# Performance work log

Hardware: AMD Instinct MI355X
Metric: run time of the kernel (lower is better)

## Reference

```python
import jax, jax.numpy as jnp
import numpy as np

N = 100000   # users
E = 50000    # hyperedges per timestep
NNZ = 800000 # incidences per timestep
T = 8        # step_split
D = 64       # embed_dim


def setup_inputs() -> dict:
    key = jax.random.key(0)
    ks = jax.random.split(key, 9)
    s = 1.0 / np.sqrt(D)
    return {
        "user_emb": jax.random.normal(ks[0], (N, D), jnp.float32) * s,
        "W_conv": jax.random.normal(ks[1], (D, D), jnp.float32) * s,
        "b_conv": jnp.zeros((D,), jnp.float32),
        "fus_w1": jax.random.normal(ks[2], (D, D), jnp.float32) * s,
        "fus_b1": jnp.zeros((D,), jnp.float32),
        "fus_w2": jax.random.normal(ks[3], (D, 1), jnp.float32) * s,
        "fus_b2": jnp.zeros((1,), jnp.float32),
        "edge_nodes": jax.random.randint(ks[4], (T, NNZ), 0, N),
        "edge_hyper": jax.random.randint(ks[5], (T, NNZ), 0, E),
    }


def _hconv(h, nodes, hyper):
    # h: [N, D] transformed node feats; nodes/hyper: [NNZ] incidence list
    ones = jnp.ones((nodes.shape[0], 1), h.dtype)
    e_sum = jax.ops.segment_sum(h[nodes], hyper, num_segments=E)      # [E, D]
    e_cnt = jax.ops.segment_sum(ones, hyper, num_segments=E)          # [E, 1]
    e = e_sum / jnp.maximum(e_cnt, 1.0)
    n_sum = jax.ops.segment_sum(e[hyper], nodes, num_segments=N)      # [N, D]
    n_cnt = jax.ops.segment_sum(ones, nodes, num_segments=N)          # [N, 1]
    return n_sum / jnp.maximum(n_cnt, 1.0)


def _fuse(hidden, dy, w1, b1, w2, b2):
    emb = jnp.stack([hidden, dy], axis=0)                             # [2, N, D]
    score = jax.nn.softmax(jnp.tanh(emb @ w1 + b1) @ w2 + b2, axis=0)  # [2, N, 1]
    return jnp.sum(score * emb, axis=0)                                # [N, D]


def reference(user_emb, W_conv, b_conv, fus_w1, fus_b1, fus_w2, fus_b2,
              edge_nodes, edge_hyper):
    # Conv input is always the raw user embedding table -> per-step convs independent.
    h = jax.nn.relu(user_emb @ W_conv + b_conv)                        # [N, D]
    conv_out = jax.vmap(lambda nd, hy: _hconv(h, nd, hy))(edge_nodes, edge_hyper)  # [T, N, D]

    def step(carry, dy):
        out = _fuse(carry, dy, fus_w1, fus_b1, fus_w2, fus_b2)
        return out, None

    final, _ = jax.lax.scan(step, conv_out[0], conv_out[1:])
    return final
```

## Files before the change

kernel.cpp:

```cpp
#include <hip/hip_runtime.h>
#include <hip/hip_bf16.h>

#define N_USERS 100000
#define E_HYPER 50000
#define NNZ_E   800000
#define T_STEPS 8
#define DIM     64

#define CAP_E   64
#define CAP_N   44

#define TR_BLOCKS  1024
#define GE_BLOCKS  1563
#define GNF_BLOCKS 1563
#define ZERO_BLKS  147

#define SC_PARTS   8
#define SC_SUB     256
#define SC_BLOCKS  (SC_PARTS * SC_SUB)
#define SC_CHUNK   (NNZ_E / SC_SUB)
#define E_SLICE    (E_HYPER / SC_PARTS)
#define N_SLICE    (N_USERS / SC_PARTS)

typedef __bf16 bf16x8 __attribute__((ext_vector_type(8)));
typedef float  f32x4  __attribute__((ext_vector_type(4)));

__device__ __forceinline__ float ld_in(const void* p, size_t i, int f32)
{
    return f32 ? ((const float*)p)[i]
               : __bfloat162float(((const __hip_bfloat16*)p)[i]);
}

__device__ __forceinline__ void st_carry(void* out, float* cws, size_t i,
                                         int f, int use_ws, float v)
{
    if (f) { ((float*)out)[i] = v; return; }
    if (use_ws) { cws[i] = v; return; }
    ((__hip_bfloat16*)out)[i] = __float2bfloat16(v);
}

__global__ void k_detect(const unsigned short* __restrict__ raw, int* __restrict__ flag)
{
    __shared__ int cnt;
    if (threadIdx.x == 0) cnt = 0;
    __syncthreads();
    int c = 0;
    for (int i = threadIdx.x; i < 4096; i += blockDim.x) {
        int e = (raw[i] >> 7) & 0xFF;
        if (e > 126) c++;
    }
    atomicAdd(&cnt, c);
    __syncthreads();
    if (threadIdx.x == 0) *flag = (cnt > 64) ? 1 : 0;
}

__global__ void k_convert_params(
    const void* W, const void* b, const void* w1, const void* b1,
    const void* w2, const void* b2, const int* __restrict__ flag,
    float* __restrict__ st)
{
    int f = *flag;
    int i = blockIdx.x * blockDim.x + threadIdx.x;
    if (i < 4096)          st[i] = ld_in(W,  i,        f);
    else if (i < 4160)     st[i] = ld_in(b,  i - 4096, f);
    else if (i < 8256)     st[i] = ld_in(w1, i - 4160, f);
    else if (i < 8320)     st[i] = ld_in(b1, i - 8256, f);
    else if (i < 8384)     st[i] = ld_in(w2, i - 8320, f);
    else if (i == 8384)    st[i] = ld_in(b2, 0,        f);
}

__device__ __forceinline__ void appendE_body(
    const int* __restrict__ nodes, const int* __restrict__ hyper,
    int* __restrict__ cnt, int* __restrict__ sn_pad, int bid, int tid)
{
    int part = bid & (SC_PARTS - 1);
    int sub  = bid >> 3;
    int elo  = part * E_SLICE;
    int i0   = sub * SC_CHUNK;
    for (int i = i0 + tid; i < i0 + SC_CHUNK; i += 256) {
        int hy = hyper[i];
        if ((unsigned)(hy - elo) < (unsigned)E_SLICE) {
            int r = atomicAdd(&cnt[hy], 1);
            if (r < CAP_E) sn_pad[hy * CAP_E + r] = nodes[i];
        }
    }
}

__device__ __forceinline__ void appendN_body(
    const int* __restrict__ nodes, const int* __restrict__ hyper,
    int* __restrict__ cnt, int* __restrict__ sh_pad, int bid, int tid)
{
    int part = bid & (SC_PARTS - 1);
    int sub  = bid >> 3;
    int nlo  = part * N_SLICE;
    int i0   = sub * SC_CHUNK;
    for (int i = i0 + tid; i < i0 + SC_CHUNK; i += 256) {
        int nd = nodes[i];
        if ((unsigned)(nd - nlo) < (unsigned)N_SLICE) {
            int r = atomicAdd(&cnt[E_HYPER + nd], 1);
            if (r < CAP_N) sh_pad[nd * CAP_N + r] = hyper[i];
        }
    }
}

__device__ __forceinline__ void zero_body(int* __restrict__ buf, int b, int tid)
{
    int idx = b * 256 + tid;
    if (idx < 150000 / 4) ((int4*)buf)[idx] = make_int4(0, 0, 0, 0);
}

__device__ __forceinline__ void ge_body(
    const __hip_bfloat16* __restrict__ h,
    const int* __restrict__ sn_pad, const int* __restrict__ cnt_e,
    __hip_bfloat16* __restrict__ e, int bid, int tid)
{
    int lane = tid & 63;
    int wid = bid * 4 + (tid >> 6);
    int nW  = GE_BLOCKS * 4;
    for (int s0 = wid * 8; s0 < E_HYPER; s0 += nW * 8) {
        int pos[8], end8[8], cnt8[8]; float acc[8];
#pragma unroll
        for (int c = 0; c < 8; ++c) {
            int sg = s0 + c;
            int cc = (sg < E_HYPER) ? cnt_e[sg] : 0;
            cnt8[c] = cc;
            pos[c]  = sg * CAP_E;
            end8[c] = pos[c] + min(cc, CAP_E);
            acc[c]  = 0.f;
        }
        while (true) {
            bool any = false;
#pragma unroll
            for (int c = 0; c < 8; ++c) any = any || (pos[c] < end8[c]);
            if (!any) break;
            int id[8];
#pragma unroll
            for (int c = 0; c < 8; ++c)
                if (pos[c] < end8[c]) id[c] = sn_pad[pos[c]];
#pragma unroll
            for (int c = 0; c < 8; ++c)
                if (pos[c] < end8[c]) {
                    acc[c] += __bfloat162float(h[(size_t)id[c] * DIM + lane]);
                    pos[c]++;
                }
        }
#pragma unroll
        for (int c = 0; c < 8; ++c) {
            int sg = s0 + c;
            if (sg < E_HYPER)
                e[(size_t)sg * DIM + lane] =
                    __float2bfloat16(acc[c] / (float)max(cnt8[c], 1));
        }
    }
}

__device__ __forceinline__ void fu_tile(
    void* __restrict__ dout, float* __restrict__ cws,
    const float* __restrict__ dyl_t, const float* __restrict__ st,
    int f, int use_ws, int write_out, int row0, int tid)
{
    float* cf = f ? (float*)dout : (use_ws ? cws : (float*)0);
    __hip_bfloat16* cb = (__hip_bfloat16*)dout;

    int lane = tid & 63;
    int quad = lane >> 4;
    int m    = lane & 15;

    bf16x8 bw[4][2];
    float b1v[4], w2v[4];
#pragma unroll
    for (int nt = 0; nt < 4; ++nt) {
#pragma unroll
        for (int kb = 0; kb < 2; ++kb)
#pragma unroll
            for (int j = 0; j < 8; ++j) {
                int k = kb * 32 + quad * 8 + j;
                bw[nt][kb][j] = (__bf16)st[4160 + k * 64 + nt * 16 + m];
            }
        b1v[nt] = st[8256 + nt * 16 + m];
        w2v[nt] = st[8320 + nt * 16 + m];
    }

    int row = row0 + m;
    size_t base = (size_t)row * DIM;

    float hidf[2][8], dyf[2][8];
    const f32x4* dp = (const f32x4*)(dyl_t + m * 68);
    if (cf) {
        const f32x4* cp = (const f32x4*)(cf + base);
#pragma unroll
        for (int kb = 0; kb < 2; ++kb) {
            f32x4 a = cp[kb * 8 + quad * 2], b = cp[kb * 8 + quad * 2 + 1];
            f32x4 c = dp[kb * 8 + quad * 2], d = dp[kb * 8 + quad * 2 + 1];
#pragma unroll
            for (int j = 0; j < 4; ++j) {
                hidf[kb][j] = a[j]; hidf[kb][4 + j] = b[j];
                dyf[kb][j]  = c[j]; dyf[kb][4 + j]  = d[j];
            }
        }
    } else {
#pragma unroll
        for (int kb = 0; kb < 2; ++kb)
#pragma unroll
            for (int j = 0; j < 8; ++j) {
                int k = kb * 32 + quad * 8 + j;
                hidf[kb][j] = __bfloat162float(cb[base + k]);
                dyf[kb][j]  = dyl_t[m * 68 + k];
            }
    }

    bf16x8 ah[2], ad[2];
#pragma unroll
    for (int kb = 0; kb < 2; ++kb)
#pragma unroll
        for (int j = 0; j < 8; ++j) {
            ah[kb][j] = (__bf16)hidf[kb][j];
            ad[kb][j] = (__bf16)dyf[kb][j];
        }

    float zh[4] = {0.f, 0.f, 0.f, 0.f};
    float zd[4] = {0.f, 0.f, 0.f, 0.f};
#pragma unroll
    for (int nt = 0; nt < 4; ++nt) {
        f32x4 acch = {0.f, 0.f, 0.f, 0.f};
        f32x4 accd = {0.f, 0.f, 0.f, 0.f};
#pragma unroll
        for (int kb = 0; kb < 2; ++kb) {
            acch = __builtin_amdgcn_mfma_f32_16x16x32_bf16(ah[kb], bw[nt][kb], acch, 0, 0, 0);
            accd = __builtin_amdgcn_mfma_f32_16x16x32_bf16(ad[kb], bw[nt][kb], accd, 0, 0, 0);
        }
#pragma unroll
        for (int reg = 0; reg < 4; ++reg) {
            zh[reg] += tanhf(acch[reg] + b1v[nt]) * w2v[nt];
            zd[reg] += tanhf(accd[reg] + b1v[nt]) * w2v[nt];
        }
    }
    float s[4];
#pragma unroll
    for (int reg = 0; reg < 4; ++reg) {
#pragma unroll
        for (int off = 1; off < 16; off <<= 1) {
            zh[reg] += __shfl_xor(zh[reg], off, 64);
            zd[reg] += __shfl_xor(zd[reg], off, 64);
        }
        float mm = fmaxf(zh[reg], zd[reg]);
        float eh = expf(zh[reg] - mm), ed = expf(zd[reg] - mm);
        s[reg] = eh / (eh + ed);
    }
    int srcl = (m >> 2) * 16;
    float s0 = __shfl(s[0], srcl, 64), s1 = __shfl(s[1], srcl, 64);
    float s2 = __shfl(s[2], srcl, 64), s3 = __shfl(s[3], srcl, 64);
    int r3 = m & 3;
    float sv = (r3 == 0) ? s0 : (r3 == 1) ? s1 : (r3 == 2) ? s2 : s3;

    if (cf) {
        f32x4* cp = (f32x4*)(cf + base);
#pragma unroll
        for (int kb = 0; kb < 2; ++kb) {
            f32x4 v0, v1;
#pragma unroll
            for (int j = 0; j < 4; ++j) {
                v0[j] = sv * hidf[kb][j]     + (1.f - sv) * dyf[kb][j];
                v1[j] = sv * hidf[kb][4 + j] + (1.f - sv) * dyf[kb][4 + j];
            }
            cp[kb * 8 + quad * 2]     = v0;
            cp[kb * 8 + quad * 2 + 1] = v1;
            if (write_out && !f) {
#pragma unroll
                for (int j = 0; j < 4; ++j) {
                    int k = kb * 32 + quad * 8 + j;
                    cb[base + k]     = __float2bfloat16(v0[j]);
                    cb[base + k + 4] = __float2bfloat16(v1[j]);
                }
            }
        }
    } else {
#pragma unroll
        for (int kb = 0; kb < 2; ++kb)
#pragma unroll
            for (int j = 0; j < 8; ++j) {
                int k = kb * 32 + quad * 8 + j;
                float v = sv * hidf[kb][j] + (1.f - sv) * dyf[kb][j];
                cb[base + k] = __float2bfloat16(v);
            }
    }
}

__global__ __launch_bounds__(256) void k_zero2(int* __restrict__ c0, int* __restrict__ c1)
{
    if ((int)blockIdx.x < ZERO_BLKS) zero_body(c0, blockIdx.x, threadIdx.x);
    else                             zero_body(c1, blockIdx.x - ZERO_BLKS, threadIdx.x);
}

__global__ __launch_bounds__(256) void k_trans_appendE(
    const void* __restrict__ emb, const int* __restrict__ flag,
    const float* __restrict__ st, __hip_bfloat16* __restrict__ h,
    const int* __restrict__ nodes, const int* __restrict__ hyper,
    int* __restrict__ cnt, int* __restrict__ sn_pad)
{
    __shared__ float Wl[DIM * DIM];
    __shared__ float bl[DIM];
    if ((int)blockIdx.x < TR_BLOCKS) {
        for (int i = threadIdx.x; i < DIM * DIM; i += blockDim.x) Wl[i] = st[i];
        if (threadIdx.x < DIM) bl[threadIdx.x] = st[4096 + threadIdx.x];
        __syncthreads();
        int f = *flag;
        int wave = threadIdx.x >> 6, lane = threadIdx.x & 63;
        int nW = TR_BLOCKS * 4;
        for (int row = blockIdx.x * 4 + wave; row < N_USERS; row += nW) {
            size_t base = (size_t)row * DIM;
            float v = ld_in(emb, base + lane, f);
            float acc = bl[lane];
#pragma unroll
            for (int k = 0; k < DIM; ++k)
                acc += __shfl(v, k, 64) * Wl[k * DIM + lane];
            h[base + lane] = __float2bfloat16(fmaxf(acc, 0.f));
        }
    } else {
        appendE_body(nodes, hyper, cnt, sn_pad,
                     blockIdx.x - TR_BLOCKS, threadIdx.x);
    }
}

__global__ __launch_bounds__(256) void k_ge_appendN(
    const __hip_bfloat16* __restrict__ h,
    const int* __restrict__ sn_pad, const int* __restrict__ cnt_cur,
    __hip_bfloat16* __restrict__ e,
    const int* __restrict__ nodes, const int* __restrict__ hyper,
    int* __restrict__ cnt_w, int* __restrict__ sh_pad)
{
    if ((int)blockIdx.x < GE_BLOCKS)
        ge_body(h, sn_pad, cnt_cur, e, blockIdx.x, threadIdx.x);
    else
        appendN_body(nodes, hyper, cnt_w, sh_pad,
                     blockIdx.x - GE_BLOCKS, threadIdx.x);
}

__global__ __launch_bounds__(256) void k_gnfuse(
    const __hip_bfloat16* __restrict__ e,
    const int* __restrict__ sh_pad, const int* __restrict__ cnt_n,
    void* __restrict__ dout, float* __restrict__ cws,
    const float* __restrict__ st, const int* __restrict__ flag,
    int use_ws, int to_carry, int write_out,
    const int* __restrict__ nodes1, const int* __restrict__ hyper1,
    int* __restrict__ cnt_nxt, int* __restrict__ sn_pad, int nsc,
    int* __restrict__ cnt_zero, int nzero)
{
    __shared__ float dyl[4 * 16 * 68];
    int b = blockIdx.x, tid = threadIdx.x;
    if (b < GNF_BLOCKS) {
        int f = *flag;
        int lane = tid & 63, w = tid >> 6;
        int wid  = b * 4 + w;
        int row0 = wid * 16;
        if (row0 >= N_USERS) return;

        int pos[16], rem[16], cnt16[16]; float acc[16];
#pragma unroll
        for (int c = 0; c < 16; ++c) {
            int sg = row0 + c;
            int cc = (sg < N_USERS) ? cnt_n[sg] : 0;
            cnt16[c] = cc;
            pos[c]   = sg * CAP_N;
            rem[c]   = min(cc, CAP_N);
            acc[c]   = 0.f;
        }
        while (true) {
            bool any = false;
#pragma unroll
            for (int c = 0; c < 16; ++c) any = any || (rem[c] > 0);
            if (!any) break;
            int hy[16];
#pragma unroll
            for (int c = 0; c < 16; ++c)
                if (rem[c] > 0) hy[c] = sh_pad[pos[c]];
#pragma unroll
            for (int c = 0; c < 16; ++c)
                if (rem[c] > 0) {
                    acc[c] += __bfloat162float(e[(size_t)hy[c] * DIM + lane]);
                    pos[c]++; rem[c]--;
                }
        }
#pragma unroll
        for (int c = 0; c < 16; ++c) {
            int sg = row0 + c;
            if (sg < N_USERS) {
                float v = acc[c] / (float)max(cnt16[c], 1);
                if (to_carry)
                    st_carry(dout, cws, (size_t)sg * DIM + lane, f, use_ws, v);
                else
                    dyl[(w * 16 + c) * 68 + lane] = v;
            }
        }
        if (!to_carry && row0 + 16 <= N_USERS)
            fu_tile(dout, cws, dyl + w * 16 * 68, st, f, use_ws,
                    write_out, row0, tid);
    } else if (b < GNF_BLOCKS + nsc) {
        appendE_body(nodes1, hyper1, cnt_nxt, sn_pad, b - GNF_BLOCKS, tid);
    } else if (nzero) {
        zero_body(cnt_zero, b - GNF_BLOCKS - nsc, tid);
    }
}

extern "C" void kernel_launch(void* const* d_in, const int* in_sizes, int n_in,
                              void* d_out, int out_size, void* d_ws,
                              size_t ws_size, hipStream_t stream)
{
    const void* user_emb = d_in[0];
    const void* W_conv   = d_in[1];
    const void* b_conv   = d_in[2];
    const void* fus_w1   = d_in[3];
    const void* fus_b1   = d_in[4];
    const void* fus_w2   = d_in[5];
    const void* fus_b2   = d_in[6];
    const int* edge_nodes = (const int*)d_in[7];
    const int* edge_hyper = (const int*)d_in[8];

    const size_t ND = (size_t)N_USERS * DIM;

    float* ws = (float*)d_ws;
    int*   flag   = (int*)ws;
    float* st     = ws + 16;
    int*   cnts[3];
    cnts[0] = (int*)(ws + 8464);
    cnts[1] = (int*)(ws + 8464 + 150016);
    cnts[2] = (int*)(ws + 8464 + 300032);
    int*   sn_pad = (int*)(ws + 458512);
    int*   sh_pad = (int*)(ws + 3658512);
    __hip_bfloat16* e_buf = (__hip_bfloat16*)(ws + 8058512);
    __hip_bfloat16* h     = (__hip_bfloat16*)(ws + 9658512);
    float* carry_ws       = ws + 12858512;

    const size_t need_ws_carry = (12858512 + ND) * 4;
    const int use_ws = (ws_size >= need_ws_carry) ? 1 : 0;

    k_detect<<<1, 256, 0, stream>>>((const unsigned short*)user_emb, flag);
    k_convert_params<<<(8385 + 255) / 256, 256, 0, stream>>>(
        W_conv, b_conv, fus_w1, fus_b1, fus_w2, fus_b2, flag, st);

    k_zero2<<<2 * ZERO_BLKS, 256, 0, stream>>>(cnts[0], cnts[1]);
    k_trans_appendE<<<TR_BLOCKS + SC_BLOCKS, 256, 0, stream>>>(
        user_emb, flag, st, h, edge_nodes, edge_hyper, cnts[0], sn_pad);

    for (int t = 0; t < T_STEPS; ++t) {
        const int* nodes0 = edge_nodes + (size_t)t * NNZ_E;
        const int* hyper0 = edge_hyper + (size_t)t * NNZ_E;
        const int* nodes1 = edge_nodes + (size_t)(t + 1) * NNZ_E;
        const int* hyper1 = edge_hyper + (size_t)(t + 1) * NNZ_E;
        int c3 = t % 3, n3 = (t + 1) % 3, z3 = (t + 2) % 3;

        k_ge_appendN<<<GE_BLOCKS + SC_BLOCKS, 256, 0, stream>>>(
            h, sn_pad, cnts[c3], e_buf, nodes0, hyper0, cnts[c3], sh_pad);

        int nsc = (t < T_STEPS - 1) ? SC_BLOCKS : 0;
        int nz  = (t < T_STEPS - 2) ? ZERO_BLKS : 0;
        k_gnfuse<<<GNF_BLOCKS + nsc + nz, 256, 0, stream>>>(
            e_buf, sh_pad, cnts[c3] + E_HYPER,
            d_out, carry_ws, st, flag, use_ws,
            (t == 0) ? 1 : 0, (t == T_STEPS - 1) ? 1 : 0,
            nodes1, hyper1, cnts[n3], sn_pad, nsc, cnts[z3], nz);
    }
}
```

Baseline: 2.278 ms.

## Software-pipeline hyperedge gather with node gather using double-buffered edge features

Restructures the per-step schedule. Each step's node gather and fusion now runs in the same launch as the next step's hyperedge-mean gather, writing into a second edge-feature buffer. Both incidence append passes and the counter zeroing move into their own launch, and a prologue launch computes step 0's edge means. Padded bucket capacities are reduced to shrink the padded index arrays. The smaller capacities risk truncating high-degree buckets, which would give wrong results if counts exceed the caps.

```diff
diff --git a/kernel.cpp b/kernel.cpp
--- a/kernel.cpp
+++ b/kernel.cpp
@@ -7,8 +7,8 @@
 #define T_STEPS 8
 #define DIM     64
 
-#define CAP_E   64
-#define CAP_N   44
+#define CAP_E   48
+#define CAP_N   36
 
 #define TR_BLOCKS  1024
 #define GE_BLOCKS  1563
@@ -322,33 +322,35 @@
     }
 }
 
-__global__ __launch_bounds__(256) void k_ge_appendN(
-    const __hip_bfloat16* __restrict__ h,
-    const int* __restrict__ sn_pad, const int* __restrict__ cnt_cur,
-    __hip_bfloat16* __restrict__ e,
-    const int* __restrict__ nodes, const int* __restrict__ hyper,
-    int* __restrict__ cnt_w, int* __restrict__ sh_pad)
-{
-    if ((int)blockIdx.x < GE_BLOCKS)
-        ge_body(h, sn_pad, cnt_cur, e, blockIdx.x, threadIdx.x);
-    else
-        appendN_body(nodes, hyper, cnt_w, sh_pad,
-                     blockIdx.x - GE_BLOCKS, threadIdx.x);
-}
-
-__global__ __launch_bounds__(256) void k_gnfuse(
-    const __hip_bfloat16* __restrict__ e,
+__global__ __launch_bounds__(256) void k_appends(
+    const int* __restrict__ nodes0, const int* __restrict__ hyper0,
+    int* __restrict__ cnt0, int* __restrict__ sh_pad, int nan_,
+    const int* __restrict__ nodes1, const int* __restrict__ hyper1,
+    int* __restrict__ cnt1, int* __restrict__ sn_pad, int nae,
+    int* __restrict__ cnt_zero, int nz)
+{
+    int b = blockIdx.x, tid = threadIdx.x;
+    if (b < nan_)
+        appendN_body(nodes0, hyper0, cnt0, sh_pad, b, tid);
+    else if (b < nan_ + nae)
+        appendE_body(nodes1, hyper1, cnt1, sn_pad, b - nan_, tid);
+    else if (nz)
+        zero_body(cnt_zero, b - nan_ - nae, tid);
+}
+
+__global__ __launch_bounds__(256) void k_gnf_ge(
+    const __hip_bfloat16* __restrict__ e_rd,
     const int* __restrict__ sh_pad, const int* __restrict__ cnt_n,
     void* __restrict__ dout, float* __restrict__ cws,
     const float* __restrict__ st, const int* __restrict__ flag,
-    int use_ws, int to_carry, int write_out,
-    const int* __restrict__ nodes1, const int* __restrict__ hyper1,
-    int* __restrict__ cnt_nxt, int* __restrict__ sn_pad, int nsc,
-    int* __restrict__ cnt_zero, int nzero)
+    int use_ws, int to_carry, int write_out, int ngnf,
+    const __hip_bfloat16* __restrict__ h,
+    const int* __restrict__ sn_pad, const int* __restrict__ cnt_e,
+    __hip_bfloat16* __restrict__ e_wr, int nge)
 {
     __shared__ float dyl[4 * 16 * 68];
     int b = blockIdx.x, tid = threadIdx.x;
-    if (b < GNF_BLOCKS) {
+    if (b < ngnf) {
         int f = *flag;
         int lane = tid & 63, w = tid >> 6;
         int wid  = b * 4 + w;
@@ -377,7 +379,7 @@
 #pragma unroll
             for (int c = 0; c < 16; ++c)
                 if (rem[c] > 0) {
-                    acc[c] += __bfloat162float(e[(size_t)hy[c] * DIM + lane]);
+                    acc[c] += __bfloat162float(e_rd[(size_t)hy[c] * DIM + lane]);
                     pos[c]++; rem[c]--;
                 }
         }
@@ -395,10 +397,8 @@
         if (!to_carry && row0 + 16 <= N_USERS)
             fu_tile(dout, cws, dyl + w * 16 * 68, st, f, use_ws,
                     write_out, row0, tid);
-    } else if (b < GNF_BLOCKS + nsc) {
-        appendE_body(nodes1, hyper1, cnt_nxt, sn_pad, b - GNF_BLOCKS, tid);
-    } else if (nzero) {
-        zero_body(cnt_zero, b - GNF_BLOCKS - nsc, tid);
+    } else if (b < ngnf + nge) {
+        ge_body(h, sn_pad, cnt_e, e_wr, b - ngnf, tid);
     }
 }
 
@@ -426,10 +426,12 @@
     cnts[1] = (int*)(ws + 8464 + 150016);
     cnts[2] = (int*)(ws + 8464 + 300032);
     int*   sn_pad = (int*)(ws + 458512);
-    int*   sh_pad = (int*)(ws + 3658512);
-    __hip_bfloat16* e_buf = (__hip_bfloat16*)(ws + 8058512);
-    __hip_bfloat16* h     = (__hip_bfloat16*)(ws + 9658512);
-    float* carry_ws       = ws + 12858512;
+    int*   sh_pad = (int*)(ws + 2858512);
+    __hip_bfloat16* e_bufs[2];
+    e_bufs[0] = (__hip_bfloat16*)(ws + 6458512);
+    e_bufs[1] = (__hip_bfloat16*)(ws + 8058512);
+    __hip_bfloat16* h = (__hip_bfloat16*)(ws + 9658512);
+    float* carry_ws   = ws + 12858512;
 
     const size_t need_ws_carry = (12858512 + ND) * 4;
     const int use_ws = (ws_size >= need_ws_carry) ? 1 : 0;
@@ -441,6 +443,10 @@
     k_zero2<<<2 * ZERO_BLKS, 256, 0, stream>>>(cnts[0], cnts[1]);
     k_trans_appendE<<<TR_BLOCKS + SC_BLOCKS, 256, 0, stream>>>(
         user_emb, flag, st, h, edge_nodes, edge_hyper, cnts[0], sn_pad);
+    k_gnf_ge<<<GE_BLOCKS, 256, 0, stream>>>(
+        e_bufs[0], sh_pad, cnts[0] + E_HYPER, d_out, carry_ws, st, flag,
+        use_ws, 0, 0, 0 ,
+        h, sn_pad, cnts[0], e_bufs[0], GE_BLOCKS);
 
     for (int t = 0; t < T_STEPS; ++t) {
         const int* nodes0 = edge_nodes + (size_t)t * NNZ_E;
@@ -449,15 +455,19 @@
         const int* hyper1 = edge_hyper + (size_t)(t + 1) * NNZ_E;
         int c3 = t % 3, n3 = (t + 1) % 3, z3 = (t + 2) % 3;
 
-        k_ge_appendN<<<GE_BLOCKS + SC_BLOCKS, 256, 0, stream>>>(
-            h, sn_pad, cnts[c3], e_buf, nodes0, hyper0, cnts[c3], sh_pad);
-
-        int nsc = (t < T_STEPS - 1) ? SC_BLOCKS : 0;
-        int nz  = (t < T_STEPS - 2) ? ZERO_BLKS : 0;
-        k_gnfuse<<<GNF_BLOCKS + nsc + nz, 256, 0, stream>>>(
-            e_buf, sh_pad, cnts[c3] + E_HYPER,
+        int nan_ = SC_BLOCKS;
+        int nae  = (t < T_STEPS - 1) ? SC_BLOCKS : 0;
+        int nz   = (t < T_STEPS - 2) ? ZERO_BLKS : 0;
+        k_appends<<<nan_ + nae + nz, 256, 0, stream>>>(
+            nodes0, hyper0, cnts[c3], sh_pad, nan_,
+            nodes1, hyper1, cnts[n3], sn_pad, nae,
+            cnts[z3], nz);
+
+        int nge = (t < T_STEPS - 1) ? GE_BLOCKS : 0;
+        k_gnf_ge<<<GNF_BLOCKS + nge, 256, 0, stream>>>(
+            e_bufs[t & 1], sh_pad, cnts[c3] + E_HYPER,
             d_out, carry_ws, st, flag, use_ws,
-            (t == 0) ? 1 : 0, (t == T_STEPS - 1) ? 1 : 0,
-            nodes1, hyper1, cnts[n3], sn_pad, nsc, cnts[z3], nz);
-    }
-}
+            (t == 0) ? 1 : 0, (t == T_STEPS - 1) ? 1 : 0, GNF_BLOCKS,
+            h, sn_pad, cnts[n3], e_bufs[(t + 1) & 1], nge);
+    }
+}
```

Measured after the change: 2.897 ms. 1.27x slower.
